# Optimization experiments

Measured on AMD Instinct MI355X. Metric: run time of the kernel, lower is better.

Reference implementation:

```python
import jax, jax.numpy as jnp
import numpy as np

EMBED_DIM = 768
NUM_HEADS = 12
SEGMENT_LENGTHS = (2048, 4096, 8192)
DILATION_RATES = (1, 2, 4)
LN_EPS = 1e-5


def setup_inputs() -> dict:
    rng = jax.random.key(0)
    ks = jax.random.split(rng, 6)
    B, S, E = 2, 8192, EMBED_DIM
    xavier = (2.0 / (E + E)) ** 0.5  # xavier_normal std for square fan-in/out
    return {
        "query": jax.random.normal(ks[0], (B, S, E), jnp.float32),
        "key": jax.random.normal(ks[1], (B, S, E), jnp.float32),
        "value": jax.random.normal(ks[2], (B, S, E), jnp.float32),
        "qkv_w": jax.random.normal(ks[3], (3 * E, E), jnp.float32) * xavier,
        "qkv_b": jnp.zeros((3 * E,), jnp.float32),
        "ln_w": jnp.ones((E,), jnp.float32),
        "ln_b": jnp.zeros((E,), jnp.float32),
        "out_w": jax.random.normal(ks[4], (E, E), jnp.float32) * xavier,
        "out_b": jnp.zeros((E,), jnp.float32),
    }


def _dilated_attention(q, k, v):
    # q,k,v: [b, n, h, d].  Heads are partitioned across the
    # (segment_length, dilation_rate) groups; within each group the sequence
    # is split into segments of length s and subsampled with stride r at
    # offset (i % r); plain softmax attention runs inside each dilated segment.
    b, n, h, d = q.shape
    G = len(SEGMENT_LENGTHS)
    g = h // G
    scale = 1.0 / np.sqrt(d)
    out = jnp.zeros_like(q)
    for i, (s, r) in enumerate(zip(SEGMENT_LENGTHS, DILATION_RATES)):
        off = i % r
        h0, h1 = i * g, (i + 1) * g
        m = n // s
        def seg(x):
            # [b, n, g, d] -> [b, m, s/r, g, d]
            return x[:, :, h0:h1].reshape(b, m, s, g, d)[:, :, off::r]
        qi, ki, vi = seg(q), seg(k), seg(v)
        scores = jnp.einsum("bmqgd,bmkgd->bmgqk", qi, ki) * scale
        p = jax.nn.softmax(scores, axis=-1)
        xi = jnp.einsum("bmgqk,bmkgd->bmqgd", p, vi)
        seg_out = jnp.zeros((b, m, s, g, d), q.dtype).at[:, :, off::r].set(xi)
        out = out.at[:, :, h0:h1].set(seg_out.reshape(b, n, g, d))
    return out / G


def reference(query, key, value, qkv_w, qkv_b, ln_w, ln_b, out_w, out_b):
    B, S, E = query.shape
    H = NUM_HEADS
    d = E // H
    # fused QKV projection (cross-attention path of the fused projection)
    q = (query @ qkv_w[:E].T + qkv_b[:E]).reshape(B, S, H, d)
    k = (key @ qkv_w[E:2 * E].T + qkv_b[E:2 * E]).reshape(B, S, H, d)
    v = (value @ qkv_w[2 * E:].T + qkv_b[2 * E:]).reshape(B, S, H, d)
    x = _dilated_attention(q, k, v).reshape(B, S, E)
    # MAGNETO layer norm before output projection
    mu = jnp.mean(x, axis=-1, keepdims=True)
    var = jnp.mean(jnp.square(x - mu), axis=-1, keepdims=True)
    x = (x - mu) * jax.lax.rsqrt(var + LN_EPS) * ln_w + ln_b
    return x @ out_w.T + out_b
```

## Files before the change

### kernel.cpp

```cpp
#include <hip/hip_runtime.h>
#include <hip/hip_bf16.h>
#include <math.h>

typedef __bf16 bf16_t;
typedef __bf16 bf16x8 __attribute__((ext_vector_type(8)));
typedef __bf16 bf16x4 __attribute__((ext_vector_type(4)));
typedef float f32x4 __attribute__((ext_vector_type(4)));

__device__ __forceinline__ void async_ld16(const void* g, void* l) {
  __builtin_amdgcn_global_load_lds(
      (const __attribute__((address_space(1))) unsigned int*)g,
      (__attribute__((address_space(3))) unsigned int*)l, 16, 0, 0);
}

#define BATCH 2
#define SEQ   8192
#define EMB   768
#define NHEAD 12
#define HD    64
#define TOK   (BATCH*SEQ)
#define GATH_PER_B 57344

__device__ __forceinline__ int headoff(int h) {
  int g = h >> 2;
  int base = (g == 0) ? 0 : ((g == 1) ? 32768 : 49152);
  return base + (h & 3) * (8192 >> g);
}

__device__ __forceinline__ float fast_exp2(float x) {
#if __has_builtin(__builtin_amdgcn_exp2f)
  return __builtin_amdgcn_exp2f(x);
#else
  return exp2f(x);
#endif
}

__global__ __launch_bounds__(256)
void k_cast_all(const float* __restrict__ q, const float* __restrict__ k,
                const float* __restrict__ v, const float* __restrict__ qkvw,
                const float* __restrict__ outw,
                bf16_t* __restrict__ qb, bf16_t* __restrict__ kb,
                bf16_t* __restrict__ vb, bf16_t* __restrict__ wqkv,
                bf16_t* __restrict__ wout) {
  int bid = blockIdx.x;
  const float* src;
  bf16_t* dst;
  int base;
  if (bid < 6144)       { src = q;    dst = qb;   base = bid; }
  else if (bid < 12288) { src = k;    dst = kb;   base = bid - 6144; }
  else if (bid < 18432) { src = v;    dst = vb;   base = bid - 12288; }
  else if (bid < 19296) { src = qkvw; dst = wqkv; base = bid - 18432; }
  else                  { src = outw; dst = wout; base = bid - 19296; }
  int i = (base * 256 + threadIdx.x) * 8;
  float4 a = *(const float4*)(src + i);
  float4 b = *(const float4*)(src + i + 4);
  __attribute__((aligned(16))) bf16_t o[8] = {
      (bf16_t)a.x, (bf16_t)a.y, (bf16_t)a.z, (bf16_t)a.w,
      (bf16_t)b.x, (bf16_t)b.y, (bf16_t)b.z, (bf16_t)b.w};
  *(uint4*)(dst + i) = *(uint4*)o;
}

__global__ __launch_bounds__(256, 2)
void k_gemm_qkv(const bf16_t* __restrict__ qb, const bf16_t* __restrict__ kb,
                const bf16_t* __restrict__ vb, const bf16_t* __restrict__ wqkv,
                const float* __restrict__ qkv_bias,
                bf16_t* __restrict__ Qg, bf16_t* __restrict__ Kg, bf16_t* __restrict__ Vb) {
  const int N = 768, K = 768;
  int id = blockIdx.x;
  int wid = (id & 7) * 288 + (id >> 3);
  int z = wid / 768;
  int rem = wid - z * 768;
  int ytile = rem / 6;
  int xtile = rem - ytile * 6;
  int m0 = ytile * 128, n0 = xtile * 128;

  const bf16_t* A = (z == 0) ? qb : (z == 1) ? kb : vb;
  const bf16_t* W = wqkv + (size_t)z * N * K;
  const float* bias = qkv_bias + z * N;

  __shared__ __align__(16) bf16_t pool[17408];
  bf16_t (*As)[128][32] = (bf16_t(*)[128][32])pool;
  bf16_t (*Bs)[128][32] = (bf16_t(*)[128][32])(pool + 8192);

  int tid = threadIdx.x;
  int wave = tid >> 6, lane = tid & 63;
  int q = lane >> 4, c = lane & 15;
  int wm = (wave & 1) * 64, wn = (wave >> 1) * 64;

  auto stage = [&](int k0, int bsel) {
#pragma unroll
    for (int it = 0; it < 2; ++it) {
      int ch = tid + it * 256;
      int row = ch >> 2, kb8 = (ch & 3) << 3;
      async_ld16(A + (size_t)(m0 + row) * K + k0 + kb8, &As[bsel][row][kb8]);
      async_ld16(W + (size_t)(n0 + row) * K + k0 + kb8, &Bs[bsel][row][kb8]);
    }
  };

  f32x4 acc[4][4];
#pragma unroll
  for (int i = 0; i < 4; i++)
#pragma unroll
    for (int j = 0; j < 4; j++) acc[i][j] = (f32x4){0.f, 0.f, 0.f, 0.f};

  stage(0, 0);
#pragma unroll 2
  for (int kt = 0; kt < 24; ++kt) {
    int cur = kt & 1;
    __syncthreads();
    if (kt + 1 < 24) stage((kt + 1) * 32, cur ^ 1);
    bf16x8 af[4], bfr[4];
#pragma unroll
    for (int mi = 0; mi < 4; mi++) af[mi] = *(const bf16x8*)&As[cur][wm + mi * 16 + c][q * 8];
#pragma unroll
    for (int nj = 0; nj < 4; nj++) bfr[nj] = *(const bf16x8*)&Bs[cur][wn + nj * 16 + c][q * 8];
#pragma unroll
    for (int mi = 0; mi < 4; mi++)
#pragma unroll
      for (int nj = 0; nj < 4; nj++)
        acc[mi][nj] = __builtin_amdgcn_mfma_f32_16x16x32_bf16(af[mi], bfr[nj], acc[mi][nj], 0, 0, 0);
  }

  __syncthreads();
  bf16_t (*Cs)[136] = (bf16_t(*)[136])pool;
  float qscale = (z == 0) ? 0.125f * 1.44269504088896f : 1.0f;
#pragma unroll
  for (int mi = 0; mi < 4; mi++)
#pragma unroll
    for (int nj = 0; nj < 4; nj++) {
      int col = wn + nj * 16 + c;
      float bi = bias[n0 + col];
#pragma unroll
      for (int rg = 0; rg < 4; rg++) {
        int row = wm + mi * 16 + q * 4 + rg;
        Cs[row][col] = (bf16_t)((acc[mi][nj][rg] + bi) * qscale);
      }
    }
  __syncthreads();

  int row = tid >> 1, hh = tid & 1;
  if (z == 2) {
    bf16_t* dp = Vb + (size_t)(m0 + row) * N + n0 + hh * 64;
#pragma unroll
    for (int k2 = 0; k2 < 8; k2++)
      *(uint4*)(dp + k2 * 8) = *(const uint4*)&Cs[row][hh * 64 + k2 * 8];
  } else {
    bf16_t* dstq = (z == 0) ? Qg : Kg;
    int h = (n0 >> 6) + hh;
    int g2 = h >> 2;
    int rm1 = (1 << g2) - 1, sh = 11 + g2;
    int smask = (2048 << g2) - 1;
    int ho = headoff(h);
    int grow = m0 + row, bb = grow >> 13, p = grow & 8191;
    int t = (p & smask) - g2;
    if (t >= 0 && (t & rm1) == 0) {
      int jj = (p >> sh) * 2048 + (t >> g2);
      bf16_t* dp = dstq + (size_t)(bb * GATH_PER_B + ho + jj) * HD;
#pragma unroll
      for (int k2 = 0; k2 < 8; k2++)
        *(uint4*)(dp + k2 * 8) = *(const uint4*)&Cs[row][hh * 64 + k2 * 8];
    }
  }
}

__global__ __launch_bounds__(256, 2)
void k_gemm_out(const bf16_t* __restrict__ A, const bf16_t* __restrict__ W,
                const float* __restrict__ bias, float* __restrict__ C) {
  const int N = 768, K = 768;
  int id = blockIdx.x;
  int wid = (id & 7) * 96 + (id >> 3);
  int ytile = wid / 6;
  int xtile = wid - ytile * 6;
  int m0 = ytile * 128, n0 = xtile * 128;

  __shared__ bf16_t As[2][128][32];
  __shared__ bf16_t Bs[2][128][32];

  int tid = threadIdx.x;
  int wave = tid >> 6, lane = tid & 63;
  int q = lane >> 4, c = lane & 15;
  int wm = (wave & 1) * 64, wn = (wave >> 1) * 64;

  auto stage = [&](int k0, int bsel) {
#pragma unroll
    for (int it = 0; it < 2; ++it) {
      int ch = tid + it * 256;
      int row = ch >> 2, kb8 = (ch & 3) << 3;
      async_ld16(A + (size_t)(m0 + row) * K + k0 + kb8, &As[bsel][row][kb8]);
      async_ld16(W + (size_t)(n0 + row) * K + k0 + kb8, &Bs[bsel][row][kb8]);
    }
  };

  f32x4 acc[4][4];
#pragma unroll
  for (int i = 0; i < 4; i++)
#pragma unroll
    for (int j = 0; j < 4; j++) acc[i][j] = (f32x4){0.f, 0.f, 0.f, 0.f};

  stage(0, 0);
#pragma unroll 2
  for (int kt = 0; kt < 24; ++kt) {
    int cur = kt & 1;
    __syncthreads();
    if (kt + 1 < 24) stage((kt + 1) * 32, cur ^ 1);
    bf16x8 af[4], bfr[4];
#pragma unroll
    for (int mi = 0; mi < 4; mi++) af[mi] = *(const bf16x8*)&As[cur][wm + mi * 16 + c][q * 8];
#pragma unroll
    for (int nj = 0; nj < 4; nj++) bfr[nj] = *(const bf16x8*)&Bs[cur][wn + nj * 16 + c][q * 8];
#pragma unroll
    for (int mi = 0; mi < 4; mi++)
#pragma unroll
      for (int nj = 0; nj < 4; nj++)
        acc[mi][nj] = __builtin_amdgcn_mfma_f32_16x16x32_bf16(af[mi], bfr[nj], acc[mi][nj], 0, 0, 0);
  }
#pragma unroll
  for (int mi = 0; mi < 4; mi++)
#pragma unroll
    for (int nj = 0; nj < 4; nj++)
#pragma unroll
      for (int rg = 0; rg < 4; rg++) {
        int row = m0 + wm + mi * 16 + q * 4 + rg;
        int col = n0 + wn + nj * 16 + c;
        C[(size_t)row * N + col] = acc[mi][nj][rg] + bias[col];
      }
}

__global__ __launch_bounds__(256)
void k_gather_v(const bf16_t* __restrict__ Vb, bf16_t* __restrict__ Vt) {
  int u = blockIdx.x, b = blockIdx.y;
  int h, jj0;
  if (u < 512)      { h = u >> 7;              jj0 = (u & 127) * 64; }
  else if (u < 768) { int w = u - 512; h = 4 + (w >> 6); jj0 = (w & 63) * 64; }
  else              { int w = u - 768; h = 8 + (w >> 5); jj0 = (w & 31) * 64; }
  int g = h >> 2;
  int L = 8192 >> g;
  int s = 2048 << g;
  int hb = b * GATH_PER_B + headoff(h);
  int tid = threadIdx.x;

  __shared__ bf16_t tile[64][72];

#pragma unroll
  for (int it = 0; it < 2; ++it) {
    int ch = tid + it * 256;
    int rowl = ch >> 3, db = (ch & 7) << 3;
    int jj = jj0 + rowl;
    int p = (jj >> 11) * s + g + ((jj & 2047) << g);
    *(uint4*)&tile[rowl][db] = *(const uint4*)(Vb + ((size_t)(b * SEQ + p)) * EMB + h * HD + db);
  }
  __syncthreads();
  int dim = tid >> 2, sub = tid & 3;
  __attribute__((aligned(16))) bf16_t tmp[16];
#pragma unroll
  for (int sl = 0; sl < 16; sl++) {
    int t = sub * 16 + sl;
    int pos = (t & 3) * 16 + (t >> 2);
    tmp[sl] = tile[pos][dim];
  }
  size_t vdst = ((size_t)hb) * HD + (size_t)dim * L + jj0 + sub * 16;
  *(uint4*)(Vt + vdst) = *(uint4*)&tmp[0];
  *(uint4*)(Vt + vdst + 8) = *(uint4*)&tmp[8];
}

__global__ __launch_bounds__(256, 2)
void k_attn(const bf16_t* __restrict__ Qg, const bf16_t* __restrict__ Kg,
            const bf16_t* __restrict__ Vt, bf16_t* __restrict__ xattn) {
  int u = blockIdx.x;
  int seg = u % 56, qt = u / 56;
  int b = seg / 28, t = seg % 28;
  int g, h, si;
  if (t < 16)      { g = 0; h = t >> 2;              si = t & 3; }
  else if (t < 24) { g = 1; h = 4 + ((t - 16) >> 1); si = (t - 16) & 1; }
  else             { g = 2; h = 8 + (t - 24);        si = 0; }
  int L = 8192 >> g, s = 2048 << g;
  int hb = b * GATH_PER_B + headoff(h);
  int jj0 = si * 2048 + qt * 128;
  int kvbase = si * 2048;

  __shared__ bf16_t Ps[128][64];
  __shared__ bf16_t Ks[2][128][64];
  __shared__ bf16_t Vs[2][64][128];

  int tid = threadIdx.x, wave = tid >> 6, lane = tid & 63;
  int q = lane >> 4, c = lane & 15;
  int cx = c & 7;
  int wm = wave * 32;

  auto stageK = [&](int kt, int bsel) {
#pragma unroll
    for (int it = 0; it < 4; ++it) {
      int ch = tid + it * 256;
      int row = ch >> 3, pc = ch & 7, lc = pc ^ (row & 7);
      async_ld16(Kg + ((size_t)(hb + kvbase + kt * 128 + row)) * HD + lc * 8,
                 &Ks[bsel][0][0] + ch * 8);
    }
  };
  auto stageV = [&](int kt, int bsel) {
#pragma unroll
    for (int it = 0; it < 4; ++it) {
      int ch = tid + it * 256;
      int dim = ch >> 4, pc = ch & 15, lc = pc ^ (dim & 7);
      async_ld16(Vt + ((size_t)hb) * HD + (size_t)dim * L + kvbase + kt * 128 + lc * 8,
                 &Vs[bsel][0][0] + ch * 8);
    }
  };

  bf16_t* Qs = &Ps[0][0];
#pragma unroll
  for (int it = 0; it < 4; ++it) {
    int ch = tid + it * 256;
    int row = ch >> 3, pc = ch & 7, lc = pc ^ (row & 7);
    async_ld16(Qg + ((size_t)(hb + jj0 + row)) * HD + lc * 8, Qs + ch * 8);
  }
  stageK(0, 0);
  stageV(0, 0);
  __syncthreads();

  bf16x8 aq[2][2];
#pragma unroll
  for (int mi = 0; mi < 2; mi++)
#pragma unroll
    for (int kq = 0; kq < 2; kq++) {
      int pch = (kq * 4 + q) ^ cx;
      aq[mi][kq] = *(const bf16x8*)(Qs + (size_t)(wm + mi * 16 + c) * HD + pch * 8);
    }

  float lrow[2][4];
  f32x4 O[2][4];
#pragma unroll
  for (int mi = 0; mi < 2; mi++)
#pragma unroll
    for (int rg = 0; rg < 4; rg++) lrow[mi][rg] = 0.f;
#pragma unroll
  for (int mi = 0; mi < 2; mi++)
#pragma unroll
    for (int vd = 0; vd < 4; vd++) O[mi][vd] = (f32x4){0.f, 0.f, 0.f, 0.f};

#pragma unroll 2
  for (int kt = 0; kt < 16; ++kt) {
    int cur = kt & 1;
    if (kt < 15) {
      stageK(kt + 1, cur ^ 1);
      stageV(kt + 1, cur ^ 1);
    }

    f32x4 Sv[2][8];
#pragma unroll
    for (int mi = 0; mi < 2; mi++)
#pragma unroll
      for (int nj = 0; nj < 8; nj++) Sv[mi][nj] = (f32x4){0.f, 0.f, 0.f, 0.f};
#pragma unroll
    for (int kq = 0; kq < 2; kq++) {
      int pch = (kq * 4 + q) ^ cx;
      bf16x8 bk[8];
#pragma unroll
      for (int nj = 0; nj < 8; nj++) bk[nj] = *(const bf16x8*)&Ks[cur][nj * 16 + c][pch * 8];
#pragma unroll
      for (int mi = 0; mi < 2; mi++)
#pragma unroll
        for (int nj = 0; nj < 8; nj++)
          Sv[mi][nj] = __builtin_amdgcn_mfma_f32_16x16x32_bf16(aq[mi][kq], bk[nj], Sv[mi][nj], 0, 0, 0);
    }

#pragma unroll
    for (int half = 0; half < 2; ++half) {
#pragma unroll
      for (int mi = 0; mi < 2; mi++)
#pragma unroll
        for (int rg = 0; rg < 4; rg++) {
          bf16x4 p4;
          float rs = 0.f;
#pragma unroll
          for (int j = 0; j < 4; j++) {
            float p = fast_exp2(Sv[mi][half * 4 + j][rg]);
            rs += p;
            p4[j] = (bf16_t)p;
          }
          lrow[mi][rg] += rs;
          int row = wm + mi * 16 + q * 4 + rg;
          int u8 = c ^ ((row & 7) << 1);
          *(bf16x4*)((char*)&Ps[row][0] + u8 * 8) = p4;
        }
#pragma unroll
      for (int kk2 = 0; kk2 < 2; ++kk2) {
        bf16x8 ap[2], bv[4];
#pragma unroll
        for (int mi = 0; mi < 2; mi++) {
          int u8 = (kk2 * 8 + q * 2) ^ (cx << 1);
          ap[mi] = *(const bf16x8*)((char*)&Ps[wm + mi * 16 + c][0] + u8 * 8);
        }
#pragma unroll
        for (int vd = 0; vd < 4; vd++) {
          int pch = (half * 8 + kk2 * 4 + q) ^ cx;
          bv[vd] = *(const bf16x8*)&Vs[cur][vd * 16 + c][pch * 8];
        }
#pragma unroll
        for (int mi = 0; mi < 2; mi++)
#pragma unroll
          for (int vd = 0; vd < 4; vd++)
            O[mi][vd] = __builtin_amdgcn_mfma_f32_16x16x32_bf16(ap[mi], bv[vd], O[mi][vd], 0, 0, 0);
      }
    }
    __syncthreads();
  }

  const float inv3 = 1.0f / 3.0f;
#pragma unroll
  for (int mi = 0; mi < 2; mi++)
#pragma unroll
    for (int rg = 0; rg < 4; rg++) {
      float l = lrow[mi][rg];
#pragma unroll
      for (int d = 1; d < 16; d <<= 1) l += __shfl_xor(l, d, 64);
      float invl = inv3 / l;
      int jj = jj0 + wm + mi * 16 + q * 4 + rg;
      int p = si * s + g + ((jj & 2047) << g);
      size_t base = ((size_t)(b * SEQ + p)) * EMB + h * HD;
#pragma unroll
      for (int vd = 0; vd < 4; vd++)
        xattn[base + vd * 16 + c] = (bf16_t)(O[mi][vd][rg] * invl);
    }
}

__global__ __launch_bounds__(256)
void k_ln(const bf16_t* __restrict__ x, const float* __restrict__ lnw,
          const float* __restrict__ lnb, bf16_t* __restrict__ y) {
  int wave = threadIdx.x >> 6, lane = threadIdx.x & 63;
  int row = blockIdx.x * 4 + wave;
  const bf16_t* xr = x + (size_t)row * EMB + lane * 12;
  bf16x4 v4[3];
#pragma unroll
  for (int j = 0; j < 3; j++) v4[j] = *(const bf16x4*)(xr + j * 4);
  float v[12], s = 0.f, s2 = 0.f;
#pragma unroll
  for (int j = 0; j < 12; j++) {
    v[j] = (float)v4[j >> 2][j & 3];
    s += v[j];
    s2 += v[j] * v[j];
  }
#pragma unroll
  for (int d = 1; d < 64; d <<= 1) { s += __shfl_xor(s, d, 64); s2 += __shfl_xor(s2, d, 64); }
  float mu = s * (1.f / 768.f);
  float var = s2 * (1.f / 768.f) - mu * mu;
  float rstd = rsqrtf(var + 1e-5f);
  const float4* wr = (const float4*)(lnw + lane * 12);
  const float4* br = (const float4*)(lnb + lane * 12);
  bf16_t* yr = y + (size_t)row * EMB + lane * 12;
#pragma unroll
  for (int j = 0; j < 3; j++) {
    float4 w = wr[j], bb = br[j];
    bf16x4 o;
    o[0] = (bf16_t)((v[j * 4 + 0] - mu) * rstd * w.x + bb.x);
    o[1] = (bf16_t)((v[j * 4 + 1] - mu) * rstd * w.y + bb.y);
    o[2] = (bf16_t)((v[j * 4 + 2] - mu) * rstd * w.z + bb.z);
    o[3] = (bf16_t)((v[j * 4 + 3] - mu) * rstd * w.w + bb.w);
    *(bf16x4*)(yr + j * 4) = o;
  }
}

extern "C" void kernel_launch(void* const* d_in, const int* in_sizes, int n_in,
                              void* d_out, int out_size, void* d_ws, size_t ws_size,
                              hipStream_t stream) {
  const float* query = (const float*)d_in[0];
  const float* key   = (const float*)d_in[1];
  const float* value = (const float*)d_in[2];
  const float* qkv_w = (const float*)d_in[3];
  const float* qkv_b = (const float*)d_in[4];
  const float* ln_w  = (const float*)d_in[5];
  const float* ln_b  = (const float*)d_in[6];
  const float* out_w = (const float*)d_in[7];
  const float* out_b = (const float*)d_in[8];
  float* out = (float*)d_out;

  char* ws = (char*)d_ws;
  const size_t A = (size_t)TOK * EMB * 2;
  bf16_t* qb    = (bf16_t*)(ws + 0 * A);
  bf16_t* kb    = (bf16_t*)(ws + 1 * A);
  bf16_t* vb    = (bf16_t*)(ws + 2 * A);
  bf16_t* Vb    = (bf16_t*)(ws + 3 * A);
  bf16_t* Qg    = (bf16_t*)(ws + 4 * A);
  bf16_t* Kg    = (bf16_t*)(ws + 5 * A);
  bf16_t* wqkv  = (bf16_t*)(ws + 6 * A);
  bf16_t* wout  = (bf16_t*)(ws + 6 * A + (size_t)2304 * 768 * 2);
  bf16_t* Vt    = vb;
  bf16_t* xattn = qb;
  bf16_t* xnorm = kb;

  k_cast_all<<<19584, 256, 0, stream>>>(query, key, value, qkv_w, out_w,
                                        qb, kb, vb, wqkv, wout);

  k_gemm_qkv<<<2304, 256, 0, stream>>>(qb, kb, vb, wqkv, qkv_b, Qg, Kg, Vb);

  dim3 gg(896, 2);
  k_gather_v<<<gg, 256, 0, stream>>>(Vb, Vt);

  hipMemsetAsync(xattn, 0, A, stream);
  k_attn<<<896, 256, 0, stream>>>(Qg, Kg, Vt, xattn);

  k_ln<<<4096, 256, 0, stream>>>(xattn, ln_w, ln_b, xnorm);

  k_gemm_out<<<768, 256, 0, stream>>>(xnorm, wout, out_b, out);
}
```

Before: 406.9 us.

## Triple-buffer GEMM K-loop with explicit vmcnt waits and barriers

Result: no change. 405.4 us (-0.4%).

```diff
diff --git a/kernel.cpp b/kernel.cpp
--- a/kernel.cpp
+++ b/kernel.cpp
@@ -34,6 +34,15 @@
   return exp2f(x);
 #endif
 }
+
+#define PIPE_SYNC(N)                                          \
+  do {                                                        \
+    __builtin_amdgcn_sched_barrier(0);                        \
+    asm volatile("s_waitcnt vmcnt(" #N ")" ::: "memory");     \
+    __builtin_amdgcn_sched_barrier(0);                        \
+    __builtin_amdgcn_s_barrier();                             \
+    __builtin_amdgcn_sched_barrier(0);                        \
+  } while (0)
 
 __global__ __launch_bounds__(256)
 void k_cast_all(const float* __restrict__ q, const float* __restrict__ k,
@@ -78,9 +87,9 @@
   const bf16_t* W = wqkv + (size_t)z * N * K;
   const float* bias = qkv_bias + z * N;
 
-  __shared__ __align__(16) bf16_t pool[17408];
+  __shared__ __align__(16) bf16_t pool[24576];
   bf16_t (*As)[128][32] = (bf16_t(*)[128][32])pool;
-  bf16_t (*Bs)[128][32] = (bf16_t(*)[128][32])(pool + 8192);
+  bf16_t (*Bs)[128][32] = (bf16_t(*)[128][32])(pool + 12288);
 
   int tid = threadIdx.x;
   int wave = tid >> 6, lane = tid & 63;
@@ -103,23 +112,29 @@
 #pragma unroll
     for (int j = 0; j < 4; j++) acc[i][j] = (f32x4){0.f, 0.f, 0.f, 0.f};
 
-  stage(0, 0);
-#pragma unroll 2
-  for (int kt = 0; kt < 24; ++kt) {
-    int cur = kt & 1;
-    __syncthreads();
-    if (kt + 1 < 24) stage((kt + 1) * 32, cur ^ 1);
+  auto compute = [&](int bsel) {
     bf16x8 af[4], bfr[4];
 #pragma unroll
-    for (int mi = 0; mi < 4; mi++) af[mi] = *(const bf16x8*)&As[cur][wm + mi * 16 + c][q * 8];
-#pragma unroll
-    for (int nj = 0; nj < 4; nj++) bfr[nj] = *(const bf16x8*)&Bs[cur][wn + nj * 16 + c][q * 8];
+    for (int mi = 0; mi < 4; mi++) af[mi] = *(const bf16x8*)&As[bsel][wm + mi * 16 + c][q * 8];
+#pragma unroll
+    for (int nj = 0; nj < 4; nj++) bfr[nj] = *(const bf16x8*)&Bs[bsel][wn + nj * 16 + c][q * 8];
 #pragma unroll
     for (int mi = 0; mi < 4; mi++)
 #pragma unroll
       for (int nj = 0; nj < 4; nj++)
         acc[mi][nj] = __builtin_amdgcn_mfma_f32_16x16x32_bf16(af[mi], bfr[nj], acc[mi][nj], 0, 0, 0);
-  }
+  };
+
+  stage(0, 0);
+  stage(32, 1);
+#pragma unroll 3
+  for (int kt = 0; kt < 23; ++kt) {
+    PIPE_SYNC(4);
+    if (kt < 22) stage((kt + 2) * 32, (kt + 2) % 3);
+    compute(kt % 3);
+  }
+  PIPE_SYNC(0);
+  compute(23 % 3);
 
   __syncthreads();
   bf16_t (*Cs)[136] = (bf16_t(*)[136])pool;
@@ -173,8 +188,8 @@
   int xtile = wid - ytile * 6;
   int m0 = ytile * 128, n0 = xtile * 128;
 
-  __shared__ bf16_t As[2][128][32];
-  __shared__ bf16_t Bs[2][128][32];
+  __shared__ bf16_t As[3][128][32];
+  __shared__ bf16_t Bs[3][128][32];
 
   int tid = threadIdx.x;
   int wave = tid >> 6, lane = tid & 63;
@@ -197,23 +212,30 @@
 #pragma unroll
     for (int j = 0; j < 4; j++) acc[i][j] = (f32x4){0.f, 0.f, 0.f, 0.f};
 
-  stage(0, 0);
-#pragma unroll 2
-  for (int kt = 0; kt < 24; ++kt) {
-    int cur = kt & 1;
-    __syncthreads();
-    if (kt + 1 < 24) stage((kt + 1) * 32, cur ^ 1);
+  auto compute = [&](int bsel) {
     bf16x8 af[4], bfr[4];
 #pragma unroll
-    for (int mi = 0; mi < 4; mi++) af[mi] = *(const bf16x8*)&As[cur][wm + mi * 16 + c][q * 8];
-#pragma unroll
-    for (int nj = 0; nj < 4; nj++) bfr[nj] = *(const bf16x8*)&Bs[cur][wn + nj * 16 + c][q * 8];
+    for (int mi = 0; mi < 4; mi++) af[mi] = *(const bf16x8*)&As[bsel][wm + mi * 16 + c][q * 8];
+#pragma unroll
+    for (int nj = 0; nj < 4; nj++) bfr[nj] = *(const bf16x8*)&Bs[bsel][wn + nj * 16 + c][q * 8];
 #pragma unroll
     for (int mi = 0; mi < 4; mi++)
 #pragma unroll
       for (int nj = 0; nj < 4; nj++)
         acc[mi][nj] = __builtin_amdgcn_mfma_f32_16x16x32_bf16(af[mi], bfr[nj], acc[mi][nj], 0, 0, 0);
-  }
+  };
+
+  stage(0, 0);
+  stage(32, 1);
+#pragma unroll 3
+  for (int kt = 0; kt < 23; ++kt) {
+    PIPE_SYNC(4);
+    if (kt < 22) stage((kt + 2) * 32, (kt + 2) % 3);
+    compute(kt % 3);
+  }
+  PIPE_SYNC(0);
+  compute(23 % 3);
+
 #pragma unroll
   for (int mi = 0; mi < 4; mi++)
 #pragma unroll
```
